# Kernel optimization log

Hardware: AMD Instinct MI355X
Metric: run time of the kernel (lower is better)

## Reference

```python
import jax, jax.numpy as jnp
import numpy as np

DIM = 512
HIDDEN = 2048
D_M = 256
R = 64
GEN_HIDDEN = D_M * 2  # hidden_mul=2
ALPHA_MEM = 1.0


def setup_inputs() -> dict:
    key = jax.random.key(0)
    ks = jax.random.split(key, 12)
    B, T = 2, 512
    inp = {
        'x': jax.random.normal(ks[0], (B, T, DIM), jnp.float32),
        'm_tok': jax.random.normal(ks[1], (B, T, D_M), jnp.float32),
        # base SwiGLU params
        'W1': jax.random.normal(ks[2], (HIDDEN, DIM), jnp.float32) * (1.0 / np.sqrt(DIM)),
        'W2': jax.random.normal(ks[3], (HIDDEN, DIM), jnp.float32) * (1.0 / np.sqrt(DIM)),
        'W3': jax.random.normal(ks[4], (DIM, HIDDEN), jnp.float32) * (1.0 / np.sqrt(HIDDEN)),
        'b1': jnp.zeros((HIDDEN,), jnp.float32),
        'b2': jnp.zeros((HIDDEN,), jnp.float32),
        'b3': jnp.zeros((DIM,), jnp.float32),
        # hypernetwork (FFNMemGenerator): d_m -> gen_hidden -> 3*r*dim
        'gen_w1': jax.random.normal(ks[5], (GEN_HIDDEN, D_M), jnp.float32) * (1.0 / np.sqrt(D_M)),
        'gen_b1': jnp.zeros((GEN_HIDDEN,), jnp.float32),
        'gen_w2': jax.random.normal(ks[6], (3 * R * DIM, GEN_HIDDEN), jnp.float32) * (0.02 / np.sqrt(GEN_HIDDEN)),
        'gen_b2': jnp.zeros((3 * R * DIM,), jnp.float32),
        'mem_gate': jnp.zeros((), jnp.float32),
    }
    return inp


def reference(x, m_tok, W1, W2, W3, b1, b2, b3, gen_w1, gen_b1, gen_w2, gen_b2, mem_gate):
    B, T, _ = x.shape
    # base SwiGLU FFN
    x1 = jnp.einsum('od,btd->bto', W1, x) + b1  # [B,T,hidden]
    x2 = jnp.einsum('od,btd->bto', W2, x) + b2
    h_base = jax.nn.silu(x1) * x2
    y_base = jnp.einsum('do,bto->btd', W3, h_base) + b3  # [B,T,dim]

    # hypernetwork-generated per-token low-rank weights
    hg = jax.nn.silu(jnp.einsum('hd,btd->bth', gen_w1, m_tok) + gen_b1)
    w = jnp.einsum('oh,bth->bto', gen_w2, hg) + gen_b2  # [B,T,3*r*dim]
    W1_m = w[..., : R * DIM].reshape(B, T, R, DIM)
    W2_m = w[..., R * DIM : 2 * R * DIM].reshape(B, T, R, DIM)
    W3_m = w[..., 2 * R * DIM :].reshape(B, T, DIM, R)

    # per-token batched matvecs (memory path)
    u1 = jnp.einsum('btrd,btd->btr', W1_m, x)
    u2 = jnp.einsum('btrd,btd->btr', W2_m, x)
    h_mem = jax.nn.silu(u1) * u2
    y_mem = jnp.einsum('btdr,btr->btd', W3_m, h_mem)

    g = jax.nn.sigmoid(mem_gate)
    return y_base + g * ALPHA_MEM * y_mem
```

## Files before the change

### kernel.cpp

```cpp
#include <hip/hip_runtime.h>
#include <cstdint>
#include <cstddef>

#define TOK   1024
#define DIMX  512
#define HID   2048
#define DM    256
#define GENH  512
#define RR    64
#define O3BASE 65536

typedef __bf16 bf16x8 __attribute__((ext_vector_type(8)));
typedef float  f32x4  __attribute__((ext_vector_type(4)));

__device__ __forceinline__ unsigned short f2bf(float f) {
  union { float f; uint32_t u; } v; v.f = f;
  return (unsigned short)((v.u + 0x7fffu + ((v.u >> 16) & 1u)) >> 16);
}
__device__ __forceinline__ float bf2f(unsigned short h) {
  union { uint32_t u; float f; } v; v.u = (uint32_t)h << 16;
  return v.f;
}
__device__ __forceinline__ float silu_f(float x) { return x / (1.f + __expf(-x)); }

__device__ __forceinline__ ushort4 cvt4_hw(float4 v) {
  union { __bf16 b; unsigned short u; } r0, r1, r2, r3;
  r0.b = (__bf16)v.x; r1.b = (__bf16)v.y; r2.b = (__bf16)v.z; r3.b = (__bf16)v.w;
  ushort4 h; h.x = r0.u; h.y = r1.u; h.z = r2.u; h.w = r3.u;
  return h;
}

__device__ __forceinline__ void async_copy16(const void* g, void* l) {
  __builtin_amdgcn_global_load_lds(
      (const __attribute__((address_space(1))) void*)g,
      (__attribute__((address_space(3))) void*)l, 16, 0, 0);
}

__device__ __forceinline__ void cast8(const float* __restrict__ src,
                                      unsigned short* __restrict__ dst, size_t i) {
  float4 v0 = *(const float4*)(src + i);
  float4 v1 = *(const float4*)(src + i + 4);
  ushort4 h0, h1;
  h0.x = f2bf(v0.x); h0.y = f2bf(v0.y); h0.z = f2bf(v0.z); h0.w = f2bf(v0.w);
  h1.x = f2bf(v1.x); h1.y = f2bf(v1.y); h1.z = f2bf(v1.z); h1.w = f2bf(v1.w);
  *(ushort4*)(dst + i)     = h0;
  *(ushort4*)(dst + i + 4) = h1;
}

template<int ROWS>
__device__ __forceinline__ void stage_tile(
    const unsigned short* __restrict__ base, size_t row0, int stride, int kofs,
    unsigned short* Ls, int tid) {
  constexpr int IT = ROWS / 32;
  const int wave = tid >> 6, lane = tid & 63;
#pragma unroll
  for (int j = 0; j < IT; ++j) {
    int s   = wave * (IT * 64) + j * 64 + lane;
    int row = s >> 3;
    int kc  = (s & 7) ^ (row & 7);
    const unsigned short* g = base + (row0 + (size_t)row) * (size_t)stride + kofs + kc * 8;
    async_copy16(g, (char*)Ls + wave * (IT * 1024) + j * 1024);
  }
}

template<int KLEN, int MF>
__device__ __forceinline__ void mfma_tile_nt(
    const unsigned short* __restrict__ Abf, size_t a_row0, int astride,
    const unsigned short* __restrict__ Bbf, size_t b_row0, int bstride, int k0,
    unsigned short* As, unsigned short* Bs, f32x4 (&acc)[MF][4]) {
  const int tid  = threadIdx.x;
  const int lane = tid & 63;
  const int wave = tid >> 6;
  const int m0 = (wave >> 1) * (MF * 16), n0 = (wave & 1) * 64;

  for (int kk = 0; kk < KLEN; kk += 64) {
    stage_tile<MF * 32>(Abf, a_row0, astride, k0 + kk, As, tid);
    stage_tile<128>(Bbf, b_row0, bstride, k0 + kk, Bs, tid);
    __syncthreads();
#pragma unroll
    for (int ks = 0; ks < 2; ++ks) {
      int cbase = ks * 4 + (lane >> 4);
      int koff  = (cbase ^ (lane & 7)) * 8;
      bf16x8 a[MF], b[4];
#pragma unroll
      for (int mf = 0; mf < MF; ++mf)
        a[mf] = *(const bf16x8*)(As + (m0 + mf * 16 + (lane & 15)) * 64 + koff);
#pragma unroll
      for (int nf = 0; nf < 4; ++nf)
        b[nf] = *(const bf16x8*)(Bs + (n0 + nf * 16 + (lane & 15)) * 64 + koff);
#pragma unroll
      for (int mf = 0; mf < MF; ++mf)
#pragma unroll
        for (int nf = 0; nf < 4; ++nf)
          acc[mf][nf] = __builtin_amdgcn_mfma_f32_16x16x32_bf16(
              a[mf], b[nf], acc[mf][nf], 0, 0, 0);
    }
    __syncthreads();
  }
}

template<int KLEN, int MF>
__device__ __forceinline__ void mfma_tile_nt_bf32(
    const unsigned short* __restrict__ Abf, size_t a_row0, int astride,
    const float* __restrict__ Bf, size_t b_row0, int bstride, int k0,
    unsigned short* As, unsigned short* Bs, f32x4 (&acc)[MF][4]) {
  const int tid  = threadIdx.x;
  const int lane = tid & 63;
  const int wave = tid >> 6;
  const int m0 = (wave >> 1) * (MF * 16), n0 = (wave & 1) * 64;

  for (int kk = 0; kk < KLEN; kk += 64) {
    stage_tile<MF * 32>(Abf, a_row0, astride, k0 + kk, As, tid);
#pragma unroll
    for (int grp = 0; grp < 2; ++grp) {
      float4 v[4];
#pragma unroll
      for (int jj = 0; jj < 2; ++jj) {
        int s   = wave * 256 + (grp * 2 + jj) * 64 + lane;
        int row = s >> 3;
        int kc  = (s & 7) ^ (row & 7);
        const float* g = Bf + (b_row0 + (size_t)row) * (size_t)bstride
                            + (k0 + kk) + kc * 8;
        v[2 * jj]     = *(const float4*)g;
        v[2 * jj + 1] = *(const float4*)(g + 4);
      }
#pragma unroll
      for (int jj = 0; jj < 2; ++jj) {
        int s = wave * 256 + (grp * 2 + jj) * 64 + lane;
        *(ushort4*)(Bs + s * 8)     = cvt4_hw(v[2 * jj]);
        *(ushort4*)(Bs + s * 8 + 4) = cvt4_hw(v[2 * jj + 1]);
      }
    }
    __syncthreads();
#pragma unroll
    for (int ks = 0; ks < 2; ++ks) {
      int cbase = ks * 4 + (lane >> 4);
      int koff  = (cbase ^ (lane & 7)) * 8;
      bf16x8 a[MF], b[4];
#pragma unroll
      for (int mf = 0; mf < MF; ++mf)
        a[mf] = *(const bf16x8*)(As + (m0 + mf * 16 + (lane & 15)) * 64 + koff);
#pragma unroll
      for (int nf = 0; nf < 4; ++nf)
        b[nf] = *(const bf16x8*)(Bs + (n0 + nf * 16 + (lane & 15)) * 64 + koff);
#pragma unroll
      for (int mf = 0; mf < MF; ++mf)
#pragma unroll
        for (int nf = 0; nf < 4; ++nf)
          acc[mf][nf] = __builtin_amdgcn_mfma_f32_16x16x32_bf16(
              a[mf], b[nf], acc[mf][nf], 0, 0, 0);
    }
    __syncthreads();
  }
}

template<int MF>
__device__ __forceinline__ void zero_accN(f32x4 (&acc)[MF][4]) {
#pragma unroll
  for (int i = 0; i < MF; ++i)
#pragma unroll
    for (int j = 0; j < 4; ++j) {
      f32x4 z = {0.f, 0.f, 0.f, 0.f};
      acc[i][j] = z;
    }
}

__global__ __launch_bounds__(256) void prep_kernel(
    const float* __restrict__ x, const float* __restrict__ m_tok,
    const float* __restrict__ gen_w1, const float* __restrict__ gen_b1,
    const float* __restrict__ W1, const float* __restrict__ W2,
    const float* __restrict__ W3,
    unsigned short* __restrict__ xb, unsigned short* __restrict__ hgb,
    unsigned short* __restrict__ W1b, unsigned short* __restrict__ W2b,
    unsigned short* __restrict__ W3b) {
  __shared__ float mt[4 * DM];
  const int tid = threadIdx.x;
  const size_t t0 = (size_t)blockIdx.x * 4;
#pragma unroll
  for (int k = 0; k < 4; ++k) mt[k * 256 + tid] = m_tok[t0 * DM + k * 256 + tid];
#pragma unroll
  for (int k = 0; k < 8; ++k) {
    size_t idx = t0 * DIMX + k * 256 + tid;
    xb[idx] = f2bf(x[idx]);
  }
  {
    size_t base = ((size_t)blockIdx.x * 256 + tid) * 8;
#pragma unroll
    for (int it = 0; it < 2; ++it) {
      size_t idx = base + (size_t)it * 524288;
      cast8(W1, W1b, idx);
      cast8(W2, W2b, idx);
      cast8(W3, W3b, idx);
    }
  }
  __syncthreads();
#pragma unroll
  for (int hh = 0; hh < 2; ++hh) {
    int h = hh * 256 + tid;
    float a0, a1, a2, a3;
    a0 = a1 = a2 = a3 = gen_b1[h];
    const float* wr = gen_w1 + (size_t)h * DM;
    for (int d = 0; d < DM; d += 4) {
      float4 w = *(const float4*)(wr + d);
      a0 += w.x * mt[d]       + w.y * mt[d + 1]       + w.z * mt[d + 2]       + w.w * mt[d + 3];
      a1 += w.x * mt[256 + d] + w.y * mt[256 + d + 1] + w.z * mt[256 + d + 2] + w.w * mt[256 + d + 3];
      a2 += w.x * mt[512 + d] + w.y * mt[512 + d + 1] + w.z * mt[512 + d + 2] + w.w * mt[512 + d + 3];
      a3 += w.x * mt[768 + d] + w.y * mt[768 + d + 1] + w.z * mt[768 + d + 2] + w.w * mt[768 + d + 3];
    }
    hgb[(t0 + 0) * GENH + h] = f2bf(silu_f(a0));
    hgb[(t0 + 1) * GENH + h] = f2bf(silu_f(a1));
    hgb[(t0 + 2) * GENH + h] = f2bf(silu_f(a2));
    hgb[(t0 + 3) * GENH + h] = f2bf(silu_f(a3));
  }
}

__device__ __forceinline__ void ffn12_body(
    int bx, const unsigned short* __restrict__ xb, const unsigned short* __restrict__ W1b,
    const unsigned short* __restrict__ W2b, const float* __restrict__ pb1,
    const float* __restrict__ pb2, unsigned short* __restrict__ hb,
    unsigned short* As, unsigned short* B1s, unsigned short* B2s) {
  const int tid = threadIdx.x, lane = tid & 63, wave = tid >> 6;
  const int ob = bx & 15, tb = bx >> 4;
  const size_t t0 = (size_t)tb * 32, o0 = (size_t)ob * 128;
  const int m0 = (wave >> 1) * 16, n0 = (wave & 1) * 64;

  f32x4 acc1[4], acc2[4];
#pragma unroll
  for (int j = 0; j < 4; ++j) {
    f32x4 z = {0.f, 0.f, 0.f, 0.f};
    acc1[j] = z; acc2[j] = z;
  }

  for (int kk = 0; kk < DIMX; kk += 64) {
    stage_tile<32>(xb, t0, DIMX, kk, As, tid);
    stage_tile<128>(W1b, o0, DIMX, kk, B1s, tid);
    stage_tile<128>(W2b, o0, DIMX, kk, B2s, tid);
    __syncthreads();
#pragma unroll
    for (int ks = 0; ks < 2; ++ks) {
      int cbase = ks * 4 + (lane >> 4);
      int koff  = (cbase ^ (lane & 7)) * 8;
      bf16x8 a, b1[4], b2[4];
      a = *(const bf16x8*)(As + (m0 + (lane & 15)) * 64 + koff);
#pragma unroll
      for (int nf = 0; nf < 4; ++nf) {
        b1[nf] = *(const bf16x8*)(B1s + (n0 + nf * 16 + (lane & 15)) * 64 + koff);
        b2[nf] = *(const bf16x8*)(B2s + (n0 + nf * 16 + (lane & 15)) * 64 + koff);
      }
#pragma unroll
      for (int nf = 0; nf < 4; ++nf) {
        acc1[nf] = __builtin_amdgcn_mfma_f32_16x16x32_bf16(a, b1[nf], acc1[nf], 0, 0, 0);
        acc2[nf] = __builtin_amdgcn_mfma_f32_16x16x32_bf16(a, b2[nf], acc2[nf], 0, 0, 0);
      }
    }
    __syncthreads();
  }

  const int q = lane >> 4;
  float b1v[4], b2v[4];
#pragma unroll
  for (int nf = 0; nf < 4; ++nf) {
    b1v[nf] = pb1[o0 + n0 + nf * 16 + (lane & 15)];
    b2v[nf] = pb2[o0 + n0 + nf * 16 + (lane & 15)];
  }
#pragma unroll
  for (int nf = 0; nf < 4; ++nf)
#pragma unroll
    for (int rg = 0; rg < 4; ++rg) {
      size_t trow = t0 + m0 + q * 4 + rg;
      size_t col  = o0 + n0 + nf * 16 + (lane & 15);
      float v1 = acc1[nf][rg] + b1v[nf];
      float v2 = acc2[nf][rg] + b2v[nf];
      hb[trow * HID + col] = f2bf(silu_f(v1) * v2);
    }
}

union SmemUV {
  struct { unsigned short As[8192], Bs[8192]; } ab;
  struct { unsigned short Xs[128 * 128]; } ep;
};

__device__ __forceinline__ void memuv_body(
    int bx, const unsigned short* __restrict__ hgb, const float* __restrict__ gw2,
    const float* __restrict__ gen_b2, const unsigned short* __restrict__ xb,
    float* __restrict__ up, SmemUV& sm) {
  const int s8 = bx & 7, w = bx >> 3;
  const int tb = w & 7, strip = (w >> 3) * 8 + s8;
  const size_t o0 = (size_t)strip * 128, t0 = (size_t)tb * 128;
  const int j  = strip >> 2;
  const int d0 = (strip & 3) * 128;

  f32x4 acc[4][4];
  zero_accN<4>(acc);
  mfma_tile_nt_bf32<GENH, 4>(hgb, t0, GENH, gw2, o0, GENH, 0, sm.ab.As, sm.ab.Bs, acc);

  const int tid = threadIdx.x, lane = tid & 63, wave = tid >> 6;
#pragma unroll
  for (int i = 0; i < 8; ++i) {
    int qq = i * 256 + tid;
    int row = qq >> 4, c = qq & 15;
    const unsigned short* src = xb + (t0 + (size_t)row) * DIMX + d0 + c * 8;
    ushort4 v0 = *(const ushort4*)src;
    ushort4 v1 = *(const ushort4*)(src + 4);
    int cs = c ^ (((row >> 2) & 3) << 1);
    unsigned short* dst = sm.ep.Xs + row * 128 + cs * 8;
    *(ushort4*)dst = v0;
    *(ushort4*)(dst + 4) = v1;
  }
  __syncthreads();

  const int m0 = (wave >> 1) * 64, n0 = (wave & 1) * 64;
  const int q = lane >> 4, l15 = lane & 15;
  float gbv[4];
#pragma unroll
  for (int i = 0; i < 4; ++i)
    gbv[i] = gen_b2[o0 + n0 + i * 16 + l15];

  const int p = (strip & 3) * 2 + (wave & 1);
  float* upd = up + (size_t)p * (128 * 1024) + (size_t)j * 1024 + t0;
#pragma unroll
  for (int mf = 0; mf < 4; ++mf) {
    f32x4 vals;
#pragma unroll
    for (int rg = 0; rg < 4; ++rg) {
      int trow = m0 + mf * 16 + q * 4 + rg;
      int swz  = ((trow >> 2) & 3) << 1;
      float val = 0.f;
#pragma unroll
      for (int nf = 0; nf < 4; ++nf) {
        int col = n0 + nf * 16 + l15;
        int idx = trow * 128 + (((col >> 3) ^ swz) << 3) + (col & 7);
        val += (acc[mf][nf][rg] + gbv[nf]) * bf2f(sm.ep.Xs[idx]);
      }
      val += __shfl_xor(val, 1);
      val += __shfl_xor(val, 2);
      val += __shfl_xor(val, 4);
      val += __shfl_xor(val, 8);
      vals[rg] = val;
    }
    if (l15 == 0)
      *(f32x4*)(upd + m0 + mf * 16 + q * 4) = vals;
  }
}

union SmemK2 {
  struct { unsigned short As[32 * 64], B1s[128 * 64], B2s[128 * 64]; } f;
  SmemUV m;
};

__global__ __launch_bounds__(256) void k2_kernel(
    const unsigned short* __restrict__ xb, const unsigned short* __restrict__ W1b,
    const unsigned short* __restrict__ W2b, const float* __restrict__ b1,
    const float* __restrict__ b2, unsigned short* __restrict__ hb,
    const unsigned short* __restrict__ hgb, const float* __restrict__ gw2,
    const float* __restrict__ gen_b2, float* __restrict__ up) {
  __shared__ SmemK2 sm;
  const int bx = blockIdx.x;
  if (bx < 512)
    ffn12_body(bx, xb, W1b, W2b, b1, b2, hb, sm.f.As, sm.f.B1s, sm.f.B2s);
  else
    memuv_body(bx - 512, hgb, gw2, gen_b2, xb, up, sm.m);
}

__device__ __forceinline__ void gemm3p_body(
    int bx, const unsigned short* __restrict__ hb, const unsigned short* __restrict__ W3b,
    float* __restrict__ yp, unsigned short* As, unsigned short* Bs) {
  const int slice = bx >> 6, r6 = bx & 63;
  const int ob = r6 & 3, tb = r6 >> 2;
  const size_t o0 = (size_t)ob * 128, t0 = (size_t)tb * 64;
  const int k0 = slice * 512;
  f32x4 acc[2][4];
  zero_accN<2>(acc);
  mfma_tile_nt<512, 2>(hb, t0, HID, W3b, o0, HID, k0, As, Bs, acc);

  const int tid = threadIdx.x, lane = tid & 63, wave = tid >> 6;
  const int m0 = (wave >> 1) * 32, n0 = (wave & 1) * 64;
  float* out = yp + (size_t)slice * (TOK * DIMX);
#pragma unroll
  for (int nf = 0; nf < 4; ++nf) {
    int n = n0 + nf * 16 + (lane & 15);
#pragma unroll
    for (int mf = 0; mf < 2; ++mf) {
      int mb = m0 + mf * 16 + ((lane >> 4) << 2);
#pragma unroll
      for (int rg = 0; rg < 4; ++rg)
        out[(t0 + mb + rg) * DIMX + o0 + n] = acc[mf][nf][rg];
    }
  }
}

__device__ __forceinline__ void hmem_body(int bx, const float* __restrict__ up,
                                          float* __restrict__ hm) {
  int i = bx * 256 + threadIdx.x;
  int t = i & 1023, r = i >> 10;
  float u1 = 0.f, u2 = 0.f;
#pragma unroll
  for (int p = 0; p < 8; ++p) {
    u1 += up[(size_t)p * (128 * 1024) + (size_t)r * 1024 + t];
    u2 += up[(size_t)p * (128 * 1024) + (size_t)(64 + r) * 1024 + t];
  }
  hm[(size_t)t * RR + r] = silu_f(u1) * u2;
}

union SmemK3 {
  struct { unsigned short As[64 * 64], Bs[128 * 64]; } g;
};

__global__ __launch_bounds__(256) void k3_kernel(
    const unsigned short* __restrict__ hb, const unsigned short* __restrict__ W3b,
    float* __restrict__ yp, const float* __restrict__ up, float* __restrict__ hm) {
  __shared__ SmemK3 sm;
  const int bx = blockIdx.x;
  if (bx < 256)
    gemm3p_body(bx, hb, W3b, yp, sm.g.As, sm.g.Bs);
  else
    hmem_body(bx - 256, up, hm);
}

union SmemY {
  struct { unsigned short As[8192], Bs[8192]; } ab;
  struct { float Hs[128 * 64]; } ep;
};

__global__ __launch_bounds__(256) void memy_kernel(
    const unsigned short* __restrict__ hgb, const float* __restrict__ gw2,
    const float* __restrict__ gen_b2, const float* __restrict__ hmem,
    const float* __restrict__ yp, const float* __restrict__ b3,
    const float* __restrict__ mem_gate, float* __restrict__ y) {
  __shared__ SmemY sm;
  const int bx = blockIdx.x;
  const int s8 = bx & 7, w = bx >> 3;
  const int tb = w & 7, strip = (w >> 3) * 8 + s8;
  const size_t brow0 = (size_t)O3BASE + (size_t)strip * 128;
  const size_t t0 = (size_t)tb * 128;

  f32x4 acc[4][4];
  zero_accN<4>(acc);
  mfma_tile_nt_bf32<GENH, 4>(hgb, t0, GENH, gw2, brow0, GENH, 0, sm.ab.As, sm.ab.Bs, acc);

  const int tid = threadIdx.x, lane = tid & 63, wave = tid >> 6;
#pragma unroll
  for (int i = 0; i < 8; ++i) {
    int qq = i * 256 + tid;
    int row = qq >> 4, c = qq & 15;
    float4 v = *(const float4*)(hmem + (t0 + (size_t)row) * RR + c * 4);
    int cs = c ^ (((row >> 2) & 3) << 2);
    *(float4*)(sm.ep.Hs + row * 64 + cs * 4) = v;
  }
  __syncthreads();

  const int m0 = (wave >> 1) * 64, n0 = (wave & 1) * 64;
  const int q = lane >> 4, l15 = lane & 15;
  const float g = 1.f / (1.f + __expf(-mem_gate[0]));
  float gbv[4];
#pragma unroll
  for (int i = 0; i < 4; ++i)
    gbv[i] = gen_b2[brow0 + n0 + i * 16 + l15];

  const int d = strip * 2 + (wave & 1);
  const float b3v = b3[d];
#pragma unroll
  for (int mf = 0; mf < 4; ++mf)
#pragma unroll
    for (int rg = 0; rg < 4; ++rg) {
      int trow = m0 + mf * 16 + q * 4 + rg;
      int swz  = ((trow >> 2) & 3) << 2;
      float val = 0.f;
#pragma unroll
      for (int nf = 0; nf < 4; ++nf) {
        int r = nf * 16 + l15;
        int idx = trow * 64 + (((r >> 2) ^ swz) << 2) + (r & 3);
        val += (acc[mf][nf][rg] + gbv[nf]) * sm.ep.Hs[idx];
      }
      val += __shfl_xor(val, 1);
      val += __shfl_xor(val, 2);
      val += __shfl_xor(val, 4);
      val += __shfl_xor(val, 8);
      if (l15 == 0) {
        size_t gi = (t0 + trow) * DIMX + d;
        float base = b3v + yp[gi]
                   + yp[(size_t)1 * (TOK * DIMX) + gi]
                   + yp[(size_t)2 * (TOK * DIMX) + gi]
                   + yp[(size_t)3 * (TOK * DIMX) + gi];
        y[gi] = base + g * val;
      }
    }
}

extern "C" void kernel_launch(void* const* d_in, const int* in_sizes, int n_in,
                              void* d_out, int out_size, void* d_ws, size_t ws_size,
                              hipStream_t stream) {
  const float* x        = (const float*)d_in[0];
  const float* m_tok    = (const float*)d_in[1];
  const float* W1       = (const float*)d_in[2];
  const float* W2       = (const float*)d_in[3];
  const float* W3       = (const float*)d_in[4];
  const float* b1       = (const float*)d_in[5];
  const float* b2       = (const float*)d_in[6];
  const float* b3       = (const float*)d_in[7];
  const float* gen_w1   = (const float*)d_in[8];
  const float* gen_b1   = (const float*)d_in[9];
  const float* gen_w2   = (const float*)d_in[10];
  const float* gen_b2   = (const float*)d_in[11];
  const float* mem_gate = (const float*)d_in[12];
  float* y = (float*)d_out;

  char* ws = (char*)d_ws;
#define KB(v) ((size_t)(v) << 10)
  unsigned short* xb  = (unsigned short*)(ws);
  unsigned short* hgb = (unsigned short*)(ws + KB(1024));
  unsigned short* hb  = (unsigned short*)(ws + KB(2048));
  float* up  = (float*)(ws + KB(6144));
  float* hm  = (float*)(ws + KB(10240));
  float* yp  = (float*)(ws + KB(10752));
  unsigned short* W1b = (unsigned short*)(ws + KB(21248));
  unsigned short* W2b = (unsigned short*)(ws + KB(23296));
  unsigned short* W3b = (unsigned short*)(ws + KB(25344));
#undef KB

  prep_kernel<<<256, 256, 0, stream>>>(x, m_tok, gen_w1, gen_b1, W1, W2, W3,
                                       xb, hgb, W1b, W2b, W3b);
  k2_kernel<<<512 + 4096, 256, 0, stream>>>(xb, W1b, W2b, b1, b2, hb,
                                            hgb, gen_w2, gen_b2, up);
  k3_kernel<<<256 + 256, 256, 0, stream>>>(hb, W3b, yp, up, hm);
  memy_kernel<<<2048, 256, 0, stream>>>(hgb, gen_w2, gen_b2, hm, yp, b3,
                                        mem_gate, y);
}
```

Measured before the change: 539.7 us.

## Double-buffer fp32-weight MFMA tile loop with register prefetch of next K tile

Replaces the single-buffered hypernetwork GEMM loop with a double-buffered pipeline. The next A tile is issued asynchronously and the next fp32 B tile is loaded into registers while MFMAs run on the current buffers; the B tile is converted to bf16 and written to LDS afterward, with one barrier per iteration. This targets the global-load latency stalls in the memory-bound gen_w2 streaming. It doubles the LDS tiles, holds eight float4 in registers, and adds launch_bounds min-blocks of 2, which may force register spills or lower occupancy.

```diff
diff --git a/kernel.cpp b/kernel.cpp
--- a/kernel.cpp
+++ b/kernel.cpp
@@ -12,6 +12,7 @@
 
 typedef __bf16 bf16x8 __attribute__((ext_vector_type(8)));
 typedef float  f32x4  __attribute__((ext_vector_type(4)));
+typedef unsigned short u16x8 __attribute__((ext_vector_type(8)));
 
 __device__ __forceinline__ unsigned short f2bf(float f) {
   union { float f; uint32_t u; } v; v.f = f;
@@ -23,11 +24,14 @@
 }
 __device__ __forceinline__ float silu_f(float x) { return x / (1.f + __expf(-x)); }
 
-__device__ __forceinline__ ushort4 cvt4_hw(float4 v) {
-  union { __bf16 b; unsigned short u; } r0, r1, r2, r3;
-  r0.b = (__bf16)v.x; r1.b = (__bf16)v.y; r2.b = (__bf16)v.z; r3.b = (__bf16)v.w;
-  ushort4 h; h.x = r0.u; h.y = r1.u; h.z = r2.u; h.w = r3.u;
-  return h;
+__device__ __forceinline__ u16x8 cvt8_hw(float4 a, float4 b) {
+  union { __bf16 h; unsigned short u; } c;
+  u16x8 r;
+  c.h = (__bf16)a.x; r[0] = c.u; c.h = (__bf16)a.y; r[1] = c.u;
+  c.h = (__bf16)a.z; r[2] = c.u; c.h = (__bf16)a.w; r[3] = c.u;
+  c.h = (__bf16)b.x; r[4] = c.u; c.h = (__bf16)b.y; r[5] = c.u;
+  c.h = (__bf16)b.z; r[6] = c.u; c.h = (__bf16)b.w; r[7] = c.u;
+  return r;
 }
 
 __device__ __forceinline__ void async_copy16(const void* g, void* l) {
@@ -100,38 +104,39 @@
 }
 
 template<int KLEN, int MF>
-__device__ __forceinline__ void mfma_tile_nt_bf32(
+__device__ __forceinline__ void mfma_pipe_bf32(
     const unsigned short* __restrict__ Abf, size_t a_row0, int astride,
-    const float* __restrict__ Bf, size_t b_row0, int bstride, int k0,
+    const float* __restrict__ Bf, size_t b_row0, int bstride,
     unsigned short* As, unsigned short* Bs, f32x4 (&acc)[MF][4]) {
   const int tid  = threadIdx.x;
   const int lane = tid & 63;
   const int wave = tid >> 6;
   const int m0 = (wave >> 1) * (MF * 16), n0 = (wave & 1) * 64;
-
-  for (int kk = 0; kk < KLEN; kk += 64) {
-    stage_tile<MF * 32>(Abf, a_row0, astride, k0 + kk, As, tid);
-#pragma unroll
-    for (int grp = 0; grp < 2; ++grp) {
-      float4 v[4];
-#pragma unroll
-      for (int jj = 0; jj < 2; ++jj) {
-        int s   = wave * 256 + (grp * 2 + jj) * 64 + lane;
-        int row = s >> 3;
-        int kc  = (s & 7) ^ (row & 7);
-        const float* g = Bf + (b_row0 + (size_t)row) * (size_t)bstride
-                            + (k0 + kk) + kc * 8;
-        v[2 * jj]     = *(const float4*)g;
-        v[2 * jj + 1] = *(const float4*)(g + 4);
-      }
-#pragma unroll
-      for (int jj = 0; jj < 2; ++jj) {
-        int s = wave * 256 + (grp * 2 + jj) * 64 + lane;
-        *(ushort4*)(Bs + s * 8)     = cvt4_hw(v[2 * jj]);
-        *(ushort4*)(Bs + s * 8 + 4) = cvt4_hw(v[2 * jj + 1]);
-      }
-    }
-    __syncthreads();
+  constexpr int ABUF = MF * 32 * 64;
+  constexpr int BBUF = 128 * 64;
+  constexpr int NT   = KLEN / 64;
+
+  float4 v[8];
+
+  auto loadB = [&](int kk) {
+#pragma unroll
+    for (int jj = 0; jj < 4; ++jj) {
+      int s   = wave * 256 + jj * 64 + lane;
+      int row = s >> 3;
+      int kc  = (s & 7) ^ (row & 7);
+      const float* g = Bf + (b_row0 + (size_t)row) * (size_t)bstride + kk + kc * 8;
+      v[2 * jj]     = *(const float4*)g;
+      v[2 * jj + 1] = *(const float4*)(g + 4);
+    }
+  };
+  auto writeB = [&](unsigned short* Bd) {
+#pragma unroll
+    for (int jj = 0; jj < 4; ++jj) {
+      int s = wave * 256 + jj * 64 + lane;
+      *(u16x8*)(Bd + s * 8) = cvt8_hw(v[2 * jj], v[2 * jj + 1]);
+    }
+  };
+  auto compute = [&](const unsigned short* Ab, const unsigned short* Bb) {
 #pragma unroll
     for (int ks = 0; ks < 2; ++ks) {
       int cbase = ks * 4 + (lane >> 4);
@@ -139,10 +144,10 @@
       bf16x8 a[MF], b[4];
 #pragma unroll
       for (int mf = 0; mf < MF; ++mf)
-        a[mf] = *(const bf16x8*)(As + (m0 + mf * 16 + (lane & 15)) * 64 + koff);
+        a[mf] = *(const bf16x8*)(Ab + (m0 + mf * 16 + (lane & 15)) * 64 + koff);
 #pragma unroll
       for (int nf = 0; nf < 4; ++nf)
-        b[nf] = *(const bf16x8*)(Bs + (n0 + nf * 16 + (lane & 15)) * 64 + koff);
+        b[nf] = *(const bf16x8*)(Bb + (n0 + nf * 16 + (lane & 15)) * 64 + koff);
 #pragma unroll
       for (int mf = 0; mf < MF; ++mf)
 #pragma unroll
@@ -150,8 +155,24 @@
           acc[mf][nf] = __builtin_amdgcn_mfma_f32_16x16x32_bf16(
               a[mf], b[nf], acc[mf][nf], 0, 0, 0);
     }
+  };
+
+  stage_tile<MF * 32>(Abf, a_row0, astride, 0, As, tid);
+  loadB(0);
+  writeB(Bs);
+  __syncthreads();
+
+  int cur = 0;
+  for (int t = 0; t < NT - 1; ++t) {
+    stage_tile<MF * 32>(Abf, a_row0, astride, (t + 1) * 64, As + (cur ^ 1) * ABUF, tid);
+    loadB((t + 1) * 64);
+    compute(As + cur * ABUF, Bs + cur * BBUF);
+    writeB(Bs + (cur ^ 1) * BBUF);
     __syncthreads();
-  }
+    cur ^= 1;
+  }
+  compute(As + cur * ABUF, Bs + cur * BBUF);
+  __syncthreads();
 }
 
 template<int MF>
@@ -276,7 +297,7 @@
 }
 
 union SmemUV {
-  struct { unsigned short As[8192], Bs[8192]; } ab;
+  struct { unsigned short As[2 * 128 * 64], Bs[2 * 128 * 64]; } ab;
   struct { unsigned short Xs[128 * 128]; } ep;
 };
 
@@ -292,7 +313,7 @@
 
   f32x4 acc[4][4];
   zero_accN<4>(acc);
-  mfma_tile_nt_bf32<GENH, 4>(hgb, t0, GENH, gw2, o0, GENH, 0, sm.ab.As, sm.ab.Bs, acc);
+  mfma_pipe_bf32<GENH, 4>(hgb, t0, GENH, gw2, o0, GENH, sm.ab.As, sm.ab.Bs, acc);
 
   const int tid = threadIdx.x, lane = tid & 63, wave = tid >> 6;
 #pragma unroll
@@ -348,7 +369,7 @@
   SmemUV m;
 };
 
-__global__ __launch_bounds__(256) void k2_kernel(
+__global__ __launch_bounds__(256, 2) void k2_kernel(
     const unsigned short* __restrict__ xb, const unsigned short* __restrict__ W1b,
     const unsigned short* __restrict__ W2b, const float* __restrict__ b1,
     const float* __restrict__ b2, unsigned short* __restrict__ hb,
@@ -418,11 +439,11 @@
 }
 
 union SmemY {
-  struct { unsigned short As[8192], Bs[8192]; } ab;
+  struct { unsigned short As[2 * 128 * 64], Bs[2 * 128 * 64]; } ab;
   struct { float Hs[128 * 64]; } ep;
 };
 
-__global__ __launch_bounds__(256) void memy_kernel(
+__global__ __launch_bounds__(256, 2) void memy_kernel(
     const unsigned short* __restrict__ hgb, const float* __restrict__ gw2,
     const float* __restrict__ gen_b2, const float* __restrict__ hmem,
     const float* __restrict__ yp, const float* __restrict__ b3,
@@ -436,7 +457,7 @@
 
   f32x4 acc[4][4];
   zero_accN<4>(acc);
-  mfma_tile_nt_bf32<GENH, 4>(hgb, t0, GENH, gw2, brow0, GENH, 0, sm.ab.As, sm.ab.Bs, acc);
+  mfma_pipe_bf32<GENH, 4>(hgb, t0, GENH, gw2, brow0, GENH, sm.ab.As, sm.ab.Bs, acc);
 
   const int tid = threadIdx.x, lane = tid & 63, wave = tid >> 6;
 #pragma unroll
```

Result: no change. 542.0 us (+0.4%).
